# Performance work log

Hardware: AMD Instinct MI355X
Metric: run time of the kernel (lower is better)

## Reference

```python
import jax, jax.numpy as jnp
import numpy as np
import math

B, Q, CQ = 2, 2048, 512
H, D = 8, 64  # no_heads, c_hidden

def setup_inputs() -> dict:
    key = jax.random.key(0)
    ks = jax.random.split(key, 8)
    s = 0.02
    return {
        "q_x": jax.random.normal(ks[0], (B, Q, CQ), jnp.float32),
        "kv_x": jax.random.normal(ks[1], (B, Q, CQ), jnp.float32),
        "bias": jax.random.normal(ks[2], (B, 1, Q, Q), jnp.float32),
        "w_qkv": jax.random.normal(ks[3], (3 * H * D, CQ), jnp.float32) * s,
        "w_o": jax.random.normal(ks[4], (CQ, H * D), jnp.float32) * s,
        "b_o": jnp.zeros((CQ,), jnp.float32),
        "w_g": jax.random.normal(ks[5], (H * D, CQ), jnp.float32) * s,
        "b_g": jnp.zeros((H * D,), jnp.float32),
    }

def reference(q_x, kv_x, bias, w_qkv, w_o, b_o, w_g, b_g):
    # Fused QKV projection from q_x (kv_x is unused by the original module's _prep_qkv)
    qkv = jnp.einsum('bqc,ec->bqe', q_x, w_qkv)  # [B,Q,3*H*D]
    q, k, v = jnp.split(qkv, 3, axis=-1)
    q = q.reshape(B, Q, H, D) / math.sqrt(D)
    k = k.reshape(B, Q, H, D)
    v = v.reshape(B, Q, H, D)
    # scores + additive pairwise bias, softmax over keys
    scores = jnp.einsum('bqhd,bkhd->bhqk', q, k) + bias  # [B,H,Q,K]
    attn = jax.nn.softmax(scores, axis=-1)
    o = jnp.einsum('bhqk,bkhd->bqhd', attn, v)  # [B,Q,H,D]
    # sigmoid gating
    g = jax.nn.sigmoid(jnp.einsum('bqc,ec->bqe', q_x, w_g) + b_g).reshape(B, Q, H, D)
    o = o * g
    # output projection
    o = o.reshape(B, Q, H * D)
    return jnp.einsum('bqe,ce->bqc', o, w_o) + b_o
```

## Files before the change

### kernel.cpp

```cpp
#include <hip/hip_runtime.h>
#include <math.h>

#define B_  2
#define Q_  2048
#define CQ_ 512
#define H_  8
#define D_  64
#define M_  (B_*Q_)
#define L2E 1.44269504088896f
#define FIXOFF 12.0f

typedef __bf16 bf16;
typedef __bf16 bf16x4 __attribute__((ext_vector_type(4)));
typedef __bf16 bf16x8 __attribute__((ext_vector_type(8)));
typedef float  f32x4  __attribute__((ext_vector_type(4)));
typedef float  f32x16 __attribute__((ext_vector_type(16)));
typedef unsigned int u32x2 __attribute__((ext_vector_type(2)));

__device__ __forceinline__ void gl_lds16(const bf16* g, bf16* l) {
    __builtin_amdgcn_global_load_lds(
        (const __attribute__((address_space(1))) unsigned int*)g,
        (__attribute__((address_space(3))) unsigned int*)l, 16, 0, 0);
}

__device__ __forceinline__ unsigned int cvtpk_bf16(float lo, float hi) {
    unsigned int r;
    asm("v_cvt_pk_bf16_f32 %0, %1, %2" : "=v"(r) : "v"(lo), "v"(hi));
    return r;
}

#define S0 (4096*512)
#define S1 (1536*512)
#define S2 (512*512)
#define S3 (512*512)
#define NCV ((S0 + S1 + S2 + S3) / (256 * 8))
__global__ __launch_bounds__(256)
void convert_kernel(const float* __restrict__ qx, const float* __restrict__ wqkv,
                    const float* __restrict__ wg, const float* __restrict__ wo,
                    const float* __restrict__ bias,
                    bf16* __restrict__ qxb, bf16* __restrict__ wcat,
                    bf16* __restrict__ wob, float* __restrict__ bT)
{
    __shared__ float lds[2048];
    const int bx = blockIdx.x;
    const int t  = threadIdx.x;
    if (bx < NCV) {
        const long long e = ((long long)bx * 256 + t) * 8;
        const float* src; bf16* dst;
        if (e < S0)                { src = qx + e;                  dst = qxb + e; }
        else if (e < S0 + S1)      { src = wqkv + (e - S0);         dst = wcat + (e - S0); }
        else if (e < S0 + S1 + S2) { src = wg + (e - S0 - S1);      dst = wcat + S1 + (e - S0 - S1); }
        else                       { src = wo + (e - S0 - S1 - S2); dst = wob + (e - S0 - S1 - S2); }
        const float4 a = *(const float4*)(src);
        const float4 b = *(const float4*)(src + 4);
        bf16x8 v;
        v[0] = (bf16)a.x; v[1] = (bf16)a.y; v[2] = (bf16)a.z; v[3] = (bf16)a.w;
        v[4] = (bf16)b.x; v[5] = (bf16)b.y; v[6] = (bf16)b.z; v[7] = (bf16)b.w;
        *(bf16x8*)dst = v;
    } else {
        const int x = bx - NCV;
        const int b = x >> 11, q32 = (x >> 5) & 63, kt = x & 31;
        const int qo = t >> 3, kc = (t & 7) * 8;
        const float* src = bias + ((size_t)b * Q_ + q32 * 32 + qo) * Q_ + kt * 64 + kc;
        const float4 a = *(const float4*)src;
        const float4 c = *(const float4*)(src + 4);
        const float v[8] = {a.x, a.y, a.z, a.w, c.x, c.y, c.z, c.w};
        #pragma unroll
        for (int j2 = 0; j2 < 8; ++j2) {
            const int ko = kc + j2;
            const int i  = (ko >> 5) * 4 + ((ko >> 3) & 3);
            const int b5 = (ko >> 2) & 1;
            const int j  = ko & 3;
            lds[i * 256 + b5 * 128 + qo * 4 + j] = v[j2] * L2E;
        }
        __syncthreads();
        float* outp = bT + ((size_t)(b * 64 + q32) * 32 + kt) * 2048 + t * 8;
        *(float4*)(outp)     = *(const float4*)(lds + t * 8);
        *(float4*)(outp + 4) = *(const float4*)(lds + t * 8 + 4);
    }
}

template<int BM, int BN>
__global__ __launch_bounds__(256)
void gemm_bf16(const bf16* __restrict__ A, const bf16* __restrict__ W,
               const float* __restrict__ bvec,
               bf16* __restrict__ qb, bf16* __restrict__ kb, bf16* __restrict__ vb,
               bf16* __restrict__ gb)
{
    constexpr int MI = BM / 32, NJ = BN / 32;
    __shared__ __align__(16) bf16 As[BM * 32];
    __shared__ __align__(16) bf16 Bs[BN * 32];

    const int t = threadIdx.x;
    const int w = t >> 6, lane = t & 63;
    const int l15 = lane & 15, quad = lane >> 4;
    const int wm = w & 1, wn = w >> 1;
    const int bm = blockIdx.x * BM;
    const int bn = blockIdx.y * BN;
    const bool swapped = ((bn >> 9) != 2);

    f32x4 acc[MI][NJ] = {};

    const int rr = t >> 2;
    const int cc = (t & 3) * 8;

    for (int k0 = 0; k0 < 512; k0 += 32) {
        #pragma unroll
        for (int i = 0; i < BM / 64; ++i)
            gl_lds16(A + (size_t)(bm + i * 64 + rr) * 512 + k0 + cc,
                     As + (i * 64 + w * 16) * 32);
        #pragma unroll
        for (int i = 0; i < BN / 64; ++i)
            gl_lds16(W + (size_t)(bn + i * 64 + rr) * 512 + k0 + cc,
                     Bs + (i * 64 + w * 16) * 32);
        __asm__ volatile("s_waitcnt vmcnt(0)" ::: "memory");
        __syncthreads();

        bf16x8 af[MI], bfr[NJ];
        #pragma unroll
        for (int i = 0; i < MI; ++i)
            af[i] = *(const bf16x8*)(As + (wm * (BM / 2) + i * 16 + l15) * 32 + quad * 8);
        #pragma unroll
        for (int j = 0; j < NJ; ++j)
            bfr[j] = *(const bf16x8*)(Bs + (wn * (BN / 2) + j * 16 + l15) * 32 + quad * 8);
        if (swapped) {
            #pragma unroll
            for (int i = 0; i < MI; ++i)
                #pragma unroll
                for (int j = 0; j < NJ; ++j)
                    acc[i][j] = __builtin_amdgcn_mfma_f32_16x16x32_bf16(bfr[j], af[i], acc[i][j], 0, 0, 0);
        } else {
            #pragma unroll
            for (int i = 0; i < MI; ++i)
                #pragma unroll
                for (int j = 0; j < NJ; ++j)
                    acc[i][j] = __builtin_amdgcn_mfma_f32_16x16x32_bf16(af[i], bfr[j], acc[i][j], 0, 0, 0);
        }
        __syncthreads();
    }

    if (swapped) {
        #pragma unroll
        for (int i = 0; i < MI; ++i) {
            const int m = bm + wm * (BM / 2) + i * 16 + l15;
            const int b = m >> 11, qq = m & 2047;
            #pragma unroll
            for (int j = 0; j < NJ; ++j) {
                const int n0 = bn + wn * (BN / 2) + j * 16 + quad * 4;
                const f32x4 cv = acc[i][j];
                const int part = n0 >> 9;
                if (part == 0) {
                    const int h = (n0 >> 6) & 7, d0 = n0 & 63;
                    bf16x4 q4;
                    #pragma unroll
                    for (int r = 0; r < 4; ++r) q4[r] = (bf16)(cv[r] * (0.125f * L2E));
                    *(bf16x4*)(qb + (size_t)(b * H_ + h) * (Q_ * D_) + (size_t)qq * 64 + d0) = q4;
                } else if (part == 1) {
                    const int h = (n0 >> 6) & 7, d0 = n0 & 63;
                    const size_t off = (size_t)(b * H_ + h) * (Q_ * D_)
                        + (qq >> 6) * 4096 + ((qq >> 5) & 1) * 2048
                        + (d0 >> 4) * 512 + ((d0 >> 3) & 1) * 256
                        + (qq & 31) * 8 + (d0 & 7);
                    bf16x4 k4;
                    #pragma unroll
                    for (int r = 0; r < 4; ++r) k4[r] = (bf16)cv[r];
                    *(bf16x4*)(kb + off) = k4;
                } else {
                    const int gcol = n0 & 511;
                    const float4 bv4 = *(const float4*)(bvec + gcol);
                    bf16x4 g4;
                    g4[0] = (bf16)(1.f / (1.f + __expf(-(cv[0] + bv4.x))));
                    g4[1] = (bf16)(1.f / (1.f + __expf(-(cv[1] + bv4.y))));
                    g4[2] = (bf16)(1.f / (1.f + __expf(-(cv[2] + bv4.z))));
                    g4[3] = (bf16)(1.f / (1.f + __expf(-(cv[3] + bv4.w))));
                    *(bf16x4*)(gb + (size_t)m * 512 + gcol) = g4;
                }
            }
        }
    } else {
        #pragma unroll
        for (int i = 0; i < MI; ++i) {
            const int m0 = bm + wm * (BM / 2) + i * 16 + quad * 4;
            const int b = m0 >> 11, qq0 = m0 & 2047;
            #pragma unroll
            for (int j = 0; j < NJ; ++j) {
                const int n = bn + wn * (BN / 2) + j * 16 + l15;
                const int h = (n >> 6) & 7, d = n & 63;
                const size_t off = (size_t)(b * H_ + h) * (Q_ * D_)
                    + (qq0 >> 6) * 4096 + (d >> 5) * 2048
                    + ((qq0 & 63) >> 4) * 512 + ((qq0 >> 3) & 1) * 256
                    + (d & 31) * 8 + (qq0 & 7);
                bf16x4 v4;
                #pragma unroll
                for (int r = 0; r < 4; ++r) v4[r] = (bf16)acc[i][j][r];
                *(bf16x4*)(vb + off) = v4;
            }
        }
    }
}

__global__ __launch_bounds__(256, 3)
void attn_part(const bf16* __restrict__ qb, const bf16* __restrict__ kf,
               const bf16* __restrict__ vf, const float* __restrict__ bT,
               bf16* __restrict__ po, float2* __restrict__ ml)
{
    __shared__ __align__(16) bf16 Ks[2][4096];
    __shared__ __align__(16) bf16 Vs[2][4096];

    const int tid  = threadIdx.x;
    const int wv   = tid >> 6, lane = tid & 63;
    const int l31  = lane & 31, b5 = lane >> 5;
    const int x    = blockIdx.x;
    const int bh   = ((x & 7) << 1) | (x >> 3);
    const int b    = bh >> 3;
    const int qg   = blockIdx.y * 128 + wv * 32 + l31;
    const int ks   = blockIdx.z;
    const int t0   = ks * 11;
    const int nt   = (ks < 2) ? 11 : 10;

    const bf16* qp = qb + ((size_t)bh * Q_ + qg) * D_;
    bf16x8 bq[4];
    #pragma unroll
    for (int c = 0; c < 4; ++c)
        bq[c] = *(const bf16x8*)(qp + c * 16 + b5 * 8);

    f32x16 acc[2] = {};
    float l_run = 0.f;

    const bf16*  kfb  = kf + (size_t)bh * (Q_ * D_) + (size_t)t0 * 4096;
    const bf16*  vfb  = vf + (size_t)bh * (Q_ * D_) + (size_t)t0 * 4096;
    const int q32 = blockIdx.y * 4 + wv;
    const float* brow = bT + (((size_t)b * 64 + q32) * 32 + t0) * 2048;

    f32x4 nb[8];

    #pragma unroll
    for (int p = 0; p < 2; ++p) {
        gl_lds16(kfb + (wv * 2 + p) * 512 + lane * 8, Ks[0] + (wv * 2 + p) * 512);
        gl_lds16(vfb + (wv * 2 + p) * 512 + lane * 8, Vs[0] + (wv * 2 + p) * 512);
    }
    #pragma unroll
    for (int i = 0; i < 8; ++i)
        nb[i] = *(const f32x4*)(brow + i * 256 + lane * 4);
    __asm__ volatile("s_waitcnt vmcnt(0)" ::: "memory");
    __syncthreads();

    int cur = 0;
    #pragma unroll 1
    for (int t = 0; t < nt; ++t) {
        if (t < nt - 1) {
            const size_t off = (size_t)(t + 1) * 4096;
            #pragma unroll
            for (int p = 0; p < 2; ++p) {
                gl_lds16(kfb + off + (wv * 2 + p) * 512 + lane * 8,
                         Ks[cur ^ 1] + (wv * 2 + p) * 512);
                gl_lds16(vfb + off + (wv * 2 + p) * 512 + lane * 8,
                         Vs[cur ^ 1] + (wv * 2 + p) * 512);
            }
        }
        __asm__ volatile("" ::: "memory");

        f32x16 sv[2];
        #pragma unroll
        for (int kg = 0; kg < 2; ++kg)
            #pragma unroll
            for (int r = 0; r < 16; ++r)
                sv[kg][r] = nb[kg * 4 + (r >> 2)][r & 3];

        if (t < nt - 1) {
            const float* bnx = brow + (size_t)(t + 1) * 2048;
            #pragma unroll
            for (int i = 0; i < 8; ++i)
                nb[i] = *(const f32x4*)(bnx + i * 256 + lane * 4);
        }
        __asm__ volatile("" ::: "memory");

        const bf16* Kc = Ks[cur];
        __builtin_amdgcn_s_setprio(1);
        #pragma unroll
        for (int kg = 0; kg < 2; ++kg)
            #pragma unroll
            for (int c = 0; c < 4; ++c) {
                const bf16x8 ak = *(const bf16x8*)(Kc + kg * 2048 + c * 512 + lane * 8);
                sv[kg] = __builtin_amdgcn_mfma_f32_32x32x16_bf16(ak, bq[c], sv[kg], 0, 0, 0);
            }
        __builtin_amdgcn_s_setprio(0);

        #pragma unroll
        for (int kg = 0; kg < 2; ++kg)
            #pragma unroll
            for (int r = 0; r < 16; ++r)
                sv[kg][r] = __builtin_amdgcn_exp2f(sv[kg][r] - FIXOFF);

        float sm[16];
        #pragma unroll
        for (int r = 0; r < 16; ++r) sm[r] = sv[0][r] + sv[1][r];
        #pragma unroll
        for (int r = 0; r < 8; ++r) sm[r] += sm[r + 8];
        #pragma unroll
        for (int r = 0; r < 4; ++r) sm[r] += sm[r + 4];
        float rsum = (sm[0] + sm[1]) + (sm[2] + sm[3]);
        rsum += __shfl_xor(rsum, 32, 64);
        l_run += rsum;

        bf16x8 bp[4];
        #pragma unroll
        for (int kg = 0; kg < 2; ++kg)
            #pragma unroll
            for (int h = 0; h < 2; ++h) {
                const unsigned int u  = cvtpk_bf16(sv[kg][8 * h + 0], sv[kg][8 * h + 1]);
                const unsigned int u2 = cvtpk_bf16(sv[kg][8 * h + 2], sv[kg][8 * h + 3]);
                const unsigned int vv = cvtpk_bf16(sv[kg][8 * h + 4], sv[kg][8 * h + 5]);
                const unsigned int v2 = cvtpk_bf16(sv[kg][8 * h + 6], sv[kg][8 * h + 7]);
                const u32x2 s1 = __builtin_amdgcn_permlane32_swap(u,  vv, false, false);
                const u32x2 s2 = __builtin_amdgcn_permlane32_swap(u2, v2, false, false);
                union { unsigned int w[4]; bf16x8 v8; } pkw;
                pkw.w[0] = s1[0]; pkw.w[1] = s2[0]; pkw.w[2] = s1[1]; pkw.w[3] = s2[1];
                bp[kg * 2 + h] = pkw.v8;
            }

        const bf16* Vc = Vs[cur];
        __builtin_amdgcn_s_setprio(1);
        #pragma unroll
        for (int c4 = 0; c4 < 4; ++c4) {
            #pragma unroll
            for (int dg = 0; dg < 2; ++dg) {
                const bf16x8 av = *(const bf16x8*)(Vc + dg * 2048 + c4 * 512 + lane * 8);
                acc[dg] = __builtin_amdgcn_mfma_f32_32x32x16_bf16(av, bp[c4], acc[dg], 0, 0, 0);
            }
        }
        __builtin_amdgcn_s_setprio(0);

        __asm__ volatile("s_waitcnt vmcnt(8) lgkmcnt(0)" ::: "memory");
        __builtin_amdgcn_sched_barrier(0);
        __builtin_amdgcn_s_barrier();
        __builtin_amdgcn_sched_barrier(0);
        cur ^= 1;
    }

    const float inv = 1.f / l_run;
    const size_t pbase = ((size_t)(ks * 16 + bh) * Q_ + qg) * 64;
    #pragma unroll
    for (int dg = 0; dg < 2; ++dg)
        #pragma unroll
        for (int gi = 0; gi < 4; ++gi) {
            const int d0 = dg * 32 + gi * 8 + b5 * 4;
            bf16x4 ov;
            #pragma unroll
            for (int r = 0; r < 4; ++r)
                ov[r] = (bf16)(acc[dg][gi * 4 + r] * inv);
            *(bf16x4*)(po + pbase + d0) = ov;
        }
    if (b5 == 0)
        ml[(size_t)(ks * 16 + bh) * Q_ + qg] = make_float2(0.f, l_run);
}

__global__ __launch_bounds__(256)
void gemm_out(const bf16* __restrict__ po, const float2* __restrict__ ml,
              const bf16* __restrict__ gb, const bf16* __restrict__ W,
              const float* __restrict__ bvec, float* __restrict__ fout)
{
    constexpr int BM = 64, BN = 128, MI = BM / 32, NJ = BN / 32;
    __shared__ __align__(16) bf16 As[BM * 32];
    __shared__ __align__(16) bf16 Bs[BN * 32];

    const int t = threadIdx.x;
    const int w = t >> 6, lane = t & 63;
    const int l15 = lane & 15, quad = lane >> 4;
    const int wm = w & 1, wn = w >> 1;
    const int bm = blockIdx.x * BM;
    const int bn = blockIdx.y * BN;

    const int rr = t >> 2;
    const int cc = (t & 3) * 8;
    const int m  = bm + rr;
    const int b  = m >> 11, qq = m & 2047;

    f32x4 acc[MI][NJ] = {};

    float2 m0_, m1_, m2_;
    bf16x8 p0_, p1_, p2_, gv_;
    auto issueA = [&](int k0) {
        const int c0 = k0 + cc;
        const int h  = c0 >> 6, d8 = c0 & 63;
        const int prow = (b * 8 + h) * 2048 + qq;
        m0_ = ml[prow];
        m1_ = ml[32768 + prow];
        m2_ = ml[65536 + prow];
        p0_ = *(const bf16x8*)(po + (size_t)prow * 64 + d8);
        p1_ = *(const bf16x8*)(po + (size_t)(32768 + prow) * 64 + d8);
        p2_ = *(const bf16x8*)(po + (size_t)(65536 + prow) * 64 + d8);
        gv_ = *(const bf16x8*)(gb + (size_t)m * 512 + c0);
    };

    issueA(0);

    for (int k0 = 0; k0 < 512; k0 += 32) {
        #pragma unroll
        for (int i = 0; i < BN / 64; ++i)
            gl_lds16(W + (size_t)(bn + i * 64 + rr) * 512 + k0 + cc,
                     Bs + (i * 64 + w * 16) * 32);

        {
            const float Mx = fmaxf(fmaxf(m0_.x, m1_.x), m2_.x);
            float w0 = m0_.y * __builtin_amdgcn_exp2f(m0_.x - Mx);
            float w1 = m1_.y * __builtin_amdgcn_exp2f(m1_.x - Mx);
            float w2 = m2_.y * __builtin_amdgcn_exp2f(m2_.x - Mx);
            const float inv = 1.f / (w0 + w1 + w2);
            w0 *= inv; w1 *= inv; w2 *= inv;
            bf16x8 av;
            #pragma unroll
            for (int r = 0; r < 8; ++r)
                av[r] = (bf16)(((float)p0_[r] * w0 + (float)p1_[r] * w1 +
                                (float)p2_[r] * w2) * (float)gv_[r]);
            *(bf16x8*)(As + t * 8) = av;
        }
        __asm__ volatile("" ::: "memory");
        issueA(k0 + 32);
        __asm__ volatile("" ::: "memory");

        __asm__ volatile("s_waitcnt vmcnt(7) lgkmcnt(0)" ::: "memory");
        __builtin_amdgcn_sched_barrier(0);
        __builtin_amdgcn_s_barrier();
        __builtin_amdgcn_sched_barrier(0);

        bf16x8 af[MI], bfr[NJ];
        #pragma unroll
        for (int i = 0; i < MI; ++i)
            af[i] = *(const bf16x8*)(As + (wm * (BM / 2) + i * 16 + l15) * 32 + quad * 8);
        #pragma unroll
        for (int j = 0; j < NJ; ++j)
            bfr[j] = *(const bf16x8*)(Bs + (wn * (BN / 2) + j * 16 + l15) * 32 + quad * 8);
        #pragma unroll
        for (int i = 0; i < MI; ++i)
            #pragma unroll
            for (int j = 0; j < NJ; ++j)
                acc[i][j] = __builtin_amdgcn_mfma_f32_16x16x32_bf16(bfr[j], af[i], acc[i][j], 0, 0, 0);

        __asm__ volatile("s_waitcnt lgkmcnt(0)" ::: "memory");
        __builtin_amdgcn_sched_barrier(0);
        __builtin_amdgcn_s_barrier();
        __builtin_amdgcn_sched_barrier(0);
    }

    #pragma unroll
    for (int i = 0; i < MI; ++i) {
        const int mm = bm + wm * (BM / 2) + i * 16 + l15;
        #pragma unroll
        for (int j = 0; j < NJ; ++j) {
            const int n0 = bn + wn * (BN / 2) + j * 16 + quad * 4;
            const f32x4 cv = acc[i][j];
            float4 st;
            st.x = cv[0] + bvec[n0 + 0];
            st.y = cv[1] + bvec[n0 + 1];
            st.z = cv[2] + bvec[n0 + 2];
            st.w = cv[3] + bvec[n0 + 3];
            *(float4*)(fout + (size_t)mm * 512 + n0) = st;
        }
    }
}

extern "C" void kernel_launch(void* const* d_in, const int* in_sizes, int n_in,
                              void* d_out, int out_size, void* d_ws, size_t ws_size,
                              hipStream_t stream)
{
    const float* q_x   = (const float*)d_in[0];
    const float* bias  = (const float*)d_in[2];
    const float* w_qkv = (const float*)d_in[3];
    const float* w_o   = (const float*)d_in[4];
    const float* b_o   = (const float*)d_in[5];
    const float* w_g   = (const float*)d_in[6];
    const float* b_g   = (const float*)d_in[7];
    float* out = (float*)d_out;

    char* ws = (char*)d_ws;
    bf16*   qxb  = (bf16*)(ws);
    bf16*   wcat = (bf16*)(ws + (4u  << 20));
    bf16*   po   = (bf16*)(ws);
    bf16*   qb   = (bf16*)(ws + (16u << 20));
    bf16*   kb   = (bf16*)(ws + (20u << 20));
    bf16*   vb   = (bf16*)(ws + (24u << 20));
    bf16*   gb   = (bf16*)(ws + (28u << 20));
    bf16*   wob  = (bf16*)(ws + (36u << 20));
    float2* ml   = (float2*)(ws + (36u << 20) + (1u << 19));
    float*  bT   = (float*)(ws + (38u << 20));

    convert_kernel<<<NCV + B_ * 64 * 32, 256, 0, stream>>>(
        q_x, w_qkv, w_g, w_o, bias, qxb, wcat, wob, bT);
    gemm_bf16<128, 128><<<dim3(32, 16), 256, 0, stream>>>(
        qxb, wcat, b_g, qb, kb, vb, gb);
    attn_part<<<dim3(B_ * H_, Q_ / 128, 3), 256, 0, stream>>>(qb, kb, vb, bT, po, ml);
    gemm_out<<<dim3(64, 4), 256, 0, stream>>>(po, ml, gb, wob, b_o, out);
}
```

Before: 175.4 us.

## Fuse fp32-to-bf16 conversion into QKV/gate GEMM and merge with bias transpose kernel

Removes the separate conversion pass for q_x and the projection weights. The GEMM blocks now load fp32 directly, convert to bf16 and store into LDS, and run in the same launch as the bias transpose and w_o conversion blocks. This drops one kernel launch and the round trip of the bf16 copies through global memory. In exchange, GEMM tiles read twice the bytes per load, lose the async global-to-LDS loads, and the GEMM blocks now share one grid with the memory-bound bias blocks.

Result: slower. 182.8 us (+4.3%).

```diff
diff --git a/kernel.cpp b/kernel.cpp
--- a/kernel.cpp
+++ b/kernel.cpp
@@ -29,36 +29,144 @@
     return r;
 }
 
-#define S0 (4096*512)
-#define S1 (1536*512)
-#define S2 (512*512)
-#define S3 (512*512)
-#define NCV ((S0 + S1 + S2 + S3) / (256 * 8))
+__device__ __forceinline__ bf16x8 cvt8(const float4 a, const float4 b) {
+    bf16x8 v;
+    v[0] = (bf16)a.x; v[1] = (bf16)a.y; v[2] = (bf16)a.z; v[3] = (bf16)a.w;
+    v[4] = (bf16)b.x; v[5] = (bf16)b.y; v[6] = (bf16)b.z; v[7] = (bf16)b.w;
+    return v;
+}
+
+#define NB_GEMM 512
+#define NB_BIAS 4096
+#define NB_WO   128
 __global__ __launch_bounds__(256)
-void convert_kernel(const float* __restrict__ qx, const float* __restrict__ wqkv,
-                    const float* __restrict__ wg, const float* __restrict__ wo,
-                    const float* __restrict__ bias,
-                    bf16* __restrict__ qxb, bf16* __restrict__ wcat,
-                    bf16* __restrict__ wob, float* __restrict__ bT)
+void fused1(const float* __restrict__ qx, const float* __restrict__ wqkv,
+            const float* __restrict__ wg, const float* __restrict__ wo,
+            const float* __restrict__ bias, const float* __restrict__ bgv,
+            bf16* __restrict__ qb, bf16* __restrict__ kb, bf16* __restrict__ vb,
+            bf16* __restrict__ gb, bf16* __restrict__ wob, float* __restrict__ bT)
 {
-    __shared__ float lds[2048];
+    __shared__ __align__(16) char smem[16384];
     const int bx = blockIdx.x;
     const int t  = threadIdx.x;
-    if (bx < NCV) {
-        const long long e = ((long long)bx * 256 + t) * 8;
-        const float* src; bf16* dst;
-        if (e < S0)                { src = qx + e;                  dst = qxb + e; }
-        else if (e < S0 + S1)      { src = wqkv + (e - S0);         dst = wcat + (e - S0); }
-        else if (e < S0 + S1 + S2) { src = wg + (e - S0 - S1);      dst = wcat + S1 + (e - S0 - S1); }
-        else                       { src = wo + (e - S0 - S1 - S2); dst = wob + (e - S0 - S1 - S2); }
-        const float4 a = *(const float4*)(src);
-        const float4 b = *(const float4*)(src + 4);
-        bf16x8 v;
-        v[0] = (bf16)a.x; v[1] = (bf16)a.y; v[2] = (bf16)a.z; v[3] = (bf16)a.w;
-        v[4] = (bf16)b.x; v[5] = (bf16)b.y; v[6] = (bf16)b.z; v[7] = (bf16)b.w;
-        *(bf16x8*)dst = v;
-    } else {
-        const int x = bx - NCV;
+
+    if (bx < NB_GEMM) {
+        bf16* As = (bf16*)smem;
+        bf16* Bs = (bf16*)(smem + 8192);
+        const int w = t >> 6, lane = t & 63;
+        const int l15 = lane & 15, quad = lane >> 4;
+        const int wm = w & 1, wn = w >> 1;
+        const int bm = (bx & 31) * 128;
+        const int bn = (bx >> 5) * 128;
+        const bool swapped = ((bn >> 9) != 2);
+
+        f32x4 acc[4][4] = {};
+        const int rr = t >> 2;
+        const int cc = (t & 3) * 8;
+        const float* wsrc = (bn < 1536) ? (wqkv + (size_t)bn * 512)
+                                        : (wg + (size_t)(bn - 1536) * 512);
+
+        for (int k0 = 0; k0 < 512; k0 += 32) {
+            #pragma unroll
+            for (int i = 0; i < 2; ++i) {
+                const float* s = qx + (size_t)(bm + i * 64 + rr) * 512 + k0 + cc;
+                const float4 a0 = *(const float4*)s;
+                const float4 a1 = *(const float4*)(s + 4);
+                *(bf16x8*)(As + (i * 64 + rr) * 32 + cc) = cvt8(a0, a1);
+            }
+            #pragma unroll
+            for (int i = 0; i < 2; ++i) {
+                const float* s = wsrc + (size_t)(i * 64 + rr) * 512 + k0 + cc;
+                const float4 a0 = *(const float4*)s;
+                const float4 a1 = *(const float4*)(s + 4);
+                *(bf16x8*)(Bs + (i * 64 + rr) * 32 + cc) = cvt8(a0, a1);
+            }
+            __syncthreads();
+
+            bf16x8 af[4], bfr[4];
+            #pragma unroll
+            for (int i = 0; i < 4; ++i)
+                af[i] = *(const bf16x8*)(As + (wm * 64 + i * 16 + l15) * 32 + quad * 8);
+            #pragma unroll
+            for (int j = 0; j < 4; ++j)
+                bfr[j] = *(const bf16x8*)(Bs + (wn * 64 + j * 16 + l15) * 32 + quad * 8);
+            if (swapped) {
+                #pragma unroll
+                for (int i = 0; i < 4; ++i)
+                    #pragma unroll
+                    for (int j = 0; j < 4; ++j)
+                        acc[i][j] = __builtin_amdgcn_mfma_f32_16x16x32_bf16(bfr[j], af[i], acc[i][j], 0, 0, 0);
+            } else {
+                #pragma unroll
+                for (int i = 0; i < 4; ++i)
+                    #pragma unroll
+                    for (int j = 0; j < 4; ++j)
+                        acc[i][j] = __builtin_amdgcn_mfma_f32_16x16x32_bf16(af[i], bfr[j], acc[i][j], 0, 0, 0);
+            }
+            __syncthreads();
+        }
+
+        if (swapped) {
+            #pragma unroll
+            for (int i = 0; i < 4; ++i) {
+                const int m = bm + wm * 64 + i * 16 + l15;
+                const int b = m >> 11, qq = m & 2047;
+                #pragma unroll
+                for (int j = 0; j < 4; ++j) {
+                    const int n0 = bn + wn * 64 + j * 16 + quad * 4;
+                    const f32x4 cv = acc[i][j];
+                    const int part = n0 >> 9;
+                    if (part == 0) {
+                        const int h = (n0 >> 6) & 7, d0 = n0 & 63;
+                        bf16x4 q4;
+                        #pragma unroll
+                        for (int r = 0; r < 4; ++r) q4[r] = (bf16)(cv[r] * (0.125f * L2E));
+                        *(bf16x4*)(qb + (size_t)(b * H_ + h) * (Q_ * D_) + (size_t)qq * 64 + d0) = q4;
+                    } else if (part == 1) {
+                        const int h = (n0 >> 6) & 7, d0 = n0 & 63;
+                        const size_t off = (size_t)(b * H_ + h) * (Q_ * D_)
+                            + (qq >> 6) * 4096 + ((qq >> 5) & 1) * 2048
+                            + (d0 >> 4) * 512 + ((d0 >> 3) & 1) * 256
+                            + (qq & 31) * 8 + (d0 & 7);
+                        bf16x4 k4;
+                        #pragma unroll
+                        for (int r = 0; r < 4; ++r) k4[r] = (bf16)cv[r];
+                        *(bf16x4*)(kb + off) = k4;
+                    } else {
+                        const int gcol = n0 & 511;
+                        const float4 bv4 = *(const float4*)(bgv + gcol);
+                        bf16x4 g4;
+                        g4[0] = (bf16)(1.f / (1.f + __expf(-(cv[0] + bv4.x))));
+                        g4[1] = (bf16)(1.f / (1.f + __expf(-(cv[1] + bv4.y))));
+                        g4[2] = (bf16)(1.f / (1.f + __expf(-(cv[2] + bv4.z))));
+                        g4[3] = (bf16)(1.f / (1.f + __expf(-(cv[3] + bv4.w))));
+                        *(bf16x4*)(gb + (size_t)m * 512 + gcol) = g4;
+                    }
+                }
+            }
+        } else {
+            #pragma unroll
+            for (int i = 0; i < 4; ++i) {
+                const int m0 = bm + wm * 64 + i * 16 + quad * 4;
+                const int b = m0 >> 11, qq0 = m0 & 2047;
+                #pragma unroll
+                for (int j = 0; j < 4; ++j) {
+                    const int n = bn + wn * 64 + j * 16 + l15;
+                    const int h = (n >> 6) & 7, d = n & 63;
+                    const size_t off = (size_t)(b * H_ + h) * (Q_ * D_)
+                        + (qq0 >> 6) * 4096 + (d >> 5) * 2048
+                        + ((qq0 & 63) >> 4) * 512 + ((qq0 >> 3) & 1) * 256
+                        + (d & 31) * 8 + (qq0 & 7);
+                    bf16x4 v4;
+                    #pragma unroll
+                    for (int r = 0; r < 4; ++r) v4[r] = (bf16)acc[i][j][r];
+                    *(bf16x4*)(vb + off) = v4;
+                }
+            }
+        }
+    } else if (bx < NB_GEMM + NB_BIAS) {
+        float* flds = (float*)smem;
+        const int x = bx - NB_GEMM;
         const int b = x >> 11, q32 = (x >> 5) & 63, kt = x & 31;
         const int qo = t >> 3, kc = (t & 7) * 8;
         const float* src = bias + ((size_t)b * Q_ + q32 * 32 + qo) * Q_ + kt * 64 + kc;
@@ -71,131 +179,17 @@
             const int i  = (ko >> 5) * 4 + ((ko >> 3) & 3);
             const int b5 = (ko >> 2) & 1;
             const int j  = ko & 3;
-            lds[i * 256 + b5 * 128 + qo * 4 + j] = v[j2] * L2E;
+            flds[i * 256 + b5 * 128 + qo * 4 + j] = v[j2] * L2E;
         }
         __syncthreads();
         float* outp = bT + ((size_t)(b * 64 + q32) * 32 + kt) * 2048 + t * 8;
-        *(float4*)(outp)     = *(const float4*)(lds + t * 8);
-        *(float4*)(outp + 4) = *(const float4*)(lds + t * 8 + 4);
-    }
-}
-
-template<int BM, int BN>
-__global__ __launch_bounds__(256)
-void gemm_bf16(const bf16* __restrict__ A, const bf16* __restrict__ W,
-               const float* __restrict__ bvec,
-               bf16* __restrict__ qb, bf16* __restrict__ kb, bf16* __restrict__ vb,
-               bf16* __restrict__ gb)
-{
-    constexpr int MI = BM / 32, NJ = BN / 32;
-    __shared__ __align__(16) bf16 As[BM * 32];
-    __shared__ __align__(16) bf16 Bs[BN * 32];
-
-    const int t = threadIdx.x;
-    const int w = t >> 6, lane = t & 63;
-    const int l15 = lane & 15, quad = lane >> 4;
-    const int wm = w & 1, wn = w >> 1;
-    const int bm = blockIdx.x * BM;
-    const int bn = blockIdx.y * BN;
-    const bool swapped = ((bn >> 9) != 2);
-
-    f32x4 acc[MI][NJ] = {};
-
-    const int rr = t >> 2;
-    const int cc = (t & 3) * 8;
-
-    for (int k0 = 0; k0 < 512; k0 += 32) {
-        #pragma unroll
-        for (int i = 0; i < BM / 64; ++i)
-            gl_lds16(A + (size_t)(bm + i * 64 + rr) * 512 + k0 + cc,
-                     As + (i * 64 + w * 16) * 32);
-        #pragma unroll
-        for (int i = 0; i < BN / 64; ++i)
-            gl_lds16(W + (size_t)(bn + i * 64 + rr) * 512 + k0 + cc,
-                     Bs + (i * 64 + w * 16) * 32);
-        __asm__ volatile("s_waitcnt vmcnt(0)" ::: "memory");
-        __syncthreads();
-
-        bf16x8 af[MI], bfr[NJ];
-        #pragma unroll
-        for (int i = 0; i < MI; ++i)
-            af[i] = *(const bf16x8*)(As + (wm * (BM / 2) + i * 16 + l15) * 32 + quad * 8);
-        #pragma unroll
-        for (int j = 0; j < NJ; ++j)
-            bfr[j] = *(const bf16x8*)(Bs + (wn * (BN / 2) + j * 16 + l15) * 32 + quad * 8);
-        if (swapped) {
-            #pragma unroll
-            for (int i = 0; i < MI; ++i)
-                #pragma unroll
-                for (int j = 0; j < NJ; ++j)
-                    acc[i][j] = __builtin_amdgcn_mfma_f32_16x16x32_bf16(bfr[j], af[i], acc[i][j], 0, 0, 0);
-        } else {
-            #pragma unroll
-            for (int i = 0; i < MI; ++i)
-                #pragma unroll
-                for (int j = 0; j < NJ; ++j)
-                    acc[i][j] = __builtin_amdgcn_mfma_f32_16x16x32_bf16(af[i], bfr[j], acc[i][j], 0, 0, 0);
-        }
-        __syncthreads();
-    }
-
-    if (swapped) {
-        #pragma unroll
-        for (int i = 0; i < MI; ++i) {
-            const int m = bm + wm * (BM / 2) + i * 16 + l15;
-            const int b = m >> 11, qq = m & 2047;
-            #pragma unroll
-            for (int j = 0; j < NJ; ++j) {
-                const int n0 = bn + wn * (BN / 2) + j * 16 + quad * 4;
-                const f32x4 cv = acc[i][j];
-                const int part = n0 >> 9;
-                if (part == 0) {
-                    const int h = (n0 >> 6) & 7, d0 = n0 & 63;
-                    bf16x4 q4;
-                    #pragma unroll
-                    for (int r = 0; r < 4; ++r) q4[r] = (bf16)(cv[r] * (0.125f * L2E));
-                    *(bf16x4*)(qb + (size_t)(b * H_ + h) * (Q_ * D_) + (size_t)qq * 64 + d0) = q4;
-                } else if (part == 1) {
-                    const int h = (n0 >> 6) & 7, d0 = n0 & 63;
-                    const size_t off = (size_t)(b * H_ + h) * (Q_ * D_)
-                        + (qq >> 6) * 4096 + ((qq >> 5) & 1) * 2048
-                        + (d0 >> 4) * 512 + ((d0 >> 3) & 1) * 256
-                        + (qq & 31) * 8 + (d0 & 7);
-                    bf16x4 k4;
-                    #pragma unroll
-                    for (int r = 0; r < 4; ++r) k4[r] = (bf16)cv[r];
-                    *(bf16x4*)(kb + off) = k4;
-                } else {
-                    const int gcol = n0 & 511;
-                    const float4 bv4 = *(const float4*)(bvec + gcol);
-                    bf16x4 g4;
-                    g4[0] = (bf16)(1.f / (1.f + __expf(-(cv[0] + bv4.x))));
-                    g4[1] = (bf16)(1.f / (1.f + __expf(-(cv[1] + bv4.y))));
-                    g4[2] = (bf16)(1.f / (1.f + __expf(-(cv[2] + bv4.z))));
-                    g4[3] = (bf16)(1.f / (1.f + __expf(-(cv[3] + bv4.w))));
-                    *(bf16x4*)(gb + (size_t)m * 512 + gcol) = g4;
-                }
-            }
-        }
+        *(float4*)(outp)     = *(const float4*)(flds + t * 8);
+        *(float4*)(outp + 4) = *(const float4*)(flds + t * 8 + 4);
     } else {
-        #pragma unroll
-        for (int i = 0; i < MI; ++i) {
-            const int m0 = bm + wm * (BM / 2) + i * 16 + quad * 4;
-            const int b = m0 >> 11, qq0 = m0 & 2047;
-            #pragma unroll
-            for (int j = 0; j < NJ; ++j) {
-                const int n = bn + wn * (BN / 2) + j * 16 + l15;
-                const int h = (n >> 6) & 7, d = n & 63;
-                const size_t off = (size_t)(b * H_ + h) * (Q_ * D_)
-                    + (qq0 >> 6) * 4096 + (d >> 5) * 2048
-                    + ((qq0 & 63) >> 4) * 512 + ((qq0 >> 3) & 1) * 256
-                    + (d & 31) * 8 + (qq0 & 7);
-                bf16x4 v4;
-                #pragma unroll
-                for (int r = 0; r < 4; ++r) v4[r] = (bf16)acc[i][j][r];
-                *(bf16x4*)(vb + off) = v4;
-            }
-        }
+        const long long e = (long long)(bx - NB_GEMM - NB_BIAS) * 2048 + t * 8;
+        const float4 a = *(const float4*)(wo + e);
+        const float4 b = *(const float4*)(wo + e + 4);
+        *(bf16x8*)(wob + e) = cvt8(a, b);
     }
 }
 
@@ -474,8 +468,6 @@
     float* out = (float*)d_out;
 
     char* ws = (char*)d_ws;
-    bf16*   qxb  = (bf16*)(ws);
-    bf16*   wcat = (bf16*)(ws + (4u  << 20));
     bf16*   po   = (bf16*)(ws);
     bf16*   qb   = (bf16*)(ws + (16u << 20));
     bf16*   kb   = (bf16*)(ws + (20u << 20));
@@ -485,10 +477,8 @@
     float2* ml   = (float2*)(ws + (36u << 20) + (1u << 19));
     float*  bT   = (float*)(ws + (38u << 20));
 
-    convert_kernel<<<NCV + B_ * 64 * 32, 256, 0, stream>>>(
-        q_x, w_qkv, w_g, w_o, bias, qxb, wcat, wob, bT);
-    gemm_bf16<128, 128><<<dim3(32, 16), 256, 0, stream>>>(
-        qxb, wcat, b_g, qb, kb, vb, gb);
+    fused1<<<NB_GEMM + NB_BIAS + NB_WO, 256, 0, stream>>>(
+        q_x, w_qkv, w_g, w_o, bias, b_g, qb, kb, vb, gb, wob, bT);
     attn_part<<<dim3(B_ * H_, Q_ / 128, 3), 256, 0, stream>>>(qb, kb, vb, bT, po, ml);
     gemm_out<<<dim3(64, 4), 256, 0, stream>>>(po, ml, gb, wob, b_o, out);
 }
```
